# Kernel tuning notes

Hardware: AMD Instinct MI355X
Metric: run time of the kernel (lower is better)

Reference implementation:

```python
import jax, jax.numpy as jnp
import numpy as np

N = 4096
F_IN = 512
ALPHA = 0.2          # LeakyReLU negative slope
NEG_INF = -9e15      # mask fill used by pyGAT


def setup_inputs() -> dict:
    key = jax.random.key(0)
    ks = jax.random.split(key, 9)
    x = jax.random.normal(ks[0], (N, F_IN), dtype=jnp.float32)
    adj = (jax.random.uniform(ks[1], (N, N)) < 0.005).astype(jnp.float32)
    adj = jnp.maximum(adj, jnp.eye(N, dtype=jnp.float32))
    s = 0.05
    W1 = jax.random.normal(ks[2], (512, 8, 128), dtype=jnp.float32) * s
    a_src1 = jax.random.normal(ks[3], (8, 128), dtype=jnp.float32) * s
    a_dst1 = jax.random.normal(ks[4], (8, 128), dtype=jnp.float32) * s
    W2 = jax.random.normal(ks[5], (1024, 1, 16), dtype=jnp.float32) * s
    a_src2 = jax.random.normal(ks[6], (1, 16), dtype=jnp.float32) * s
    a_dst2 = jax.random.normal(ks[7], (1, 16), dtype=jnp.float32) * s
    return {"x": x, "adj": adj, "W1": W1, "a_src1": a_src1, "a_dst1": a_dst1,
            "W2": W2, "a_src2": a_src2, "a_dst2": a_dst2}


def gat_layer(x, mask, W, a_src, a_dst, concat, activation):
    # x: [N, Fin], W: [Fin, H, Fout]
    h = jnp.einsum('nf,fho->nho', x, W)                  # [N, H, Fout]
    f_src = jnp.einsum('nho,ho->hn', h, a_src)            # [H, N]
    f_dst = jnp.einsum('nho,ho->hn', h, a_dst)            # [H, N]
    e = f_src[:, :, None] + f_dst[:, None, :]             # [H, N, N]
    e = jax.nn.leaky_relu(e, ALPHA)
    e = jnp.where(mask[None, :, :], e, NEG_INF)
    attn = jax.nn.softmax(e, axis=-1)                     # masked softmax over neighbors j
    out = jnp.einsum('hij,jho->iho', attn, h)             # [N, H, Fout]
    if concat:
        out = out.reshape(out.shape[0], -1)               # [N, H*Fout]
    else:
        out = out.mean(axis=1)                            # [N, Fout]
    if activation:
        out = jax.nn.elu(out)
    return out


def reference(x, adj, W1, a_src1, a_dst1, W2, a_src2, a_dst2):
    mask = adj > 0
    h1 = gat_layer(x, mask, W1, a_src1, a_dst1, concat=True, activation=True)
    h2 = gat_layer(h1, mask, W2, a_src2, a_dst2, concat=False, activation=False)
    out = jax.nn.elu(h2)
    return jax.nn.log_softmax(out, axis=1)
```

## Files before the change

### kernel.cpp

```cpp
#include <hip/hip_runtime.h>
#include <hip/hip_bf16.h>
#include <hip/hip_fp16.h>

typedef __attribute__((ext_vector_type(8))) short short8;
typedef __attribute__((ext_vector_type(8))) _Float16 half8;
typedef __attribute__((ext_vector_type(2))) _Float16 h2v;
typedef __attribute__((ext_vector_type(4))) float f32x4;

#define MAXNBR 128
#define ALPHA 0.2f

static __device__ __forceinline__ unsigned short f2h(float f) {
    return __half_as_ushort(__float2half(f));
}
static __device__ __forceinline__ float h2f(unsigned short u) {
    return __half2float(__ushort_as_half(u));
}

__global__ __launch_bounds__(256) void cvt(const float* __restrict__ x,
                                           unsigned short* __restrict__ xh,
                                           const float* __restrict__ W1,
                                           unsigned short* __restrict__ W1t) {
    int b = blockIdx.x, t = threadIdx.x;
    if (b < 1024) {
        size_t base = (size_t)b * 2048 + t * 8;
        float4 v0 = *(const float4*)&x[base];
        float4 v1 = *(const float4*)&x[base + 4];
        short8 o;
        o[0] = f2h(v0.x); o[1] = f2h(v0.y); o[2] = f2h(v0.z); o[3] = f2h(v0.w);
        o[4] = f2h(v1.x); o[5] = f2h(v1.y); o[6] = f2h(v1.z); o[7] = f2h(v1.w);
        *(short8*)&xh[base] = o;
    } else {
        int idx = (b - 1024) * 256 + t;
        int c = idx >> 9, k = idx & 511;
        W1t[idx] = f2h(W1[(size_t)k * 1024 + c]);
    }
}

__global__ __launch_bounds__(256) void gemm_scan(const unsigned short* __restrict__ A,
                                                 const unsigned short* __restrict__ Bt,
                                                 unsigned short* __restrict__ C,
                                                 const float* __restrict__ adj,
                                                 int* __restrict__ nbr_idx,
                                                 int* __restrict__ nbr_cnt) {
    __shared__ unsigned short Asm[128 * 64];
    __shared__ unsigned short Bsm[64 * 64];
    int b = blockIdx.x;
    int tid = threadIdx.x;
    if (b < 512) {
        int lane = tid & 63;
        int w = tid >> 6;
        int wr = w >> 1, wc = w & 1;
        int rowBase = (b & 31) * 128, colBase = (b >> 5) * 64;
        int lr = lane >> 3;
        int lcs = ((lane & 7) ^ lr) * 8;
        f32x4 acc[4][2] = {};
        for (int k0 = 0; k0 < 512; k0 += 64) {
            #pragma unroll
            for (int i = 0; i < 4; ++i) {
                int rA = i * 32 + w * 8;
                __builtin_amdgcn_global_load_lds(
                    (const __attribute__((address_space(1))) void*)&A[(size_t)(rowBase + rA + lr) * 512 + k0 + lcs],
                    (__attribute__((address_space(3))) void*)&Asm[rA * 64],
                    16, 0, 0);
            }
            #pragma unroll
            for (int i = 0; i < 2; ++i) {
                int rB = i * 32 + w * 8;
                __builtin_amdgcn_global_load_lds(
                    (const __attribute__((address_space(1))) void*)&Bt[(size_t)(colBase + rB + lr) * 512 + k0 + lcs],
                    (__attribute__((address_space(3))) void*)&Bsm[rB * 64],
                    16, 0, 0);
            }
            __syncthreads();
            #pragma unroll
            for (int kk = 0; kk < 64; kk += 32) {
                half8 af[4], bfv[2];
                int kf = kk + (lane >> 4) * 8;
                #pragma unroll
                for (int m = 0; m < 4; ++m) {
                    int R = wr * 64 + m * 16 + (lane & 15);
                    af[m] = *(const half8*)&Asm[R * 64 + (kf ^ ((R & 7) << 3))];
                }
                #pragma unroll
                for (int n = 0; n < 2; ++n) {
                    int R = wc * 32 + n * 16 + (lane & 15);
                    bfv[n] = *(const half8*)&Bsm[R * 64 + (kf ^ ((R & 7) << 3))];
                }
                #pragma unroll
                for (int m = 0; m < 4; ++m)
                    #pragma unroll
                    for (int n = 0; n < 2; ++n)
                        acc[m][n] = __builtin_amdgcn_mfma_f32_16x16x32_f16(af[m], bfv[n], acc[m][n], 0, 0, 0);
            }
            __syncthreads();
        }
        int crow0 = rowBase + wr * 64, ccol0 = colBase + wc * 32;
        #pragma unroll
        for (int m = 0; m < 4; ++m)
            #pragma unroll
            for (int n = 0; n < 2; ++n) {
                int col = ccol0 + n * 16 + (lane & 15);
                int row0 = crow0 + m * 16 + (lane >> 4) * 4;
                #pragma unroll
                for (int r = 0; r < 4; ++r)
                    C[(size_t)(row0 + r) * 1024 + col] = f2h(acc[m][n][r]);
            }
    } else {
        int row = (b - 512) * 4 + (tid >> 6);
        int lane = tid & 63;
        const float* arow = adj + (size_t)row * 4096;
        int cnt = 0;
        for (int base = 0; base < 4096; base += 256) {
            float4 v = *(const float4*)&arow[base + lane * 4];
            #pragma unroll
            for (int s = 0; s < 4; ++s) {
                float xv = ((const float*)&v)[s];
                unsigned long long m = __ballot(xv > 0.f);
                if (xv > 0.f) {
                    int pos = cnt + (int)__popcll(m & ((1ull << lane) - 1ull));
                    if (pos < MAXNBR) nbr_idx[row * MAXNBR + pos] = base + lane * 4 + s;
                }
                cnt += (int)__popcll(m);
            }
        }
        if (lane == 0) nbr_cnt[row] = cnt < MAXNBR ? cnt : MAXNBR;
    }
}

__global__ __launch_bounds__(256) void attn_coef1(const unsigned short* __restrict__ h1h,
                                                  const float* __restrict__ a_src,
                                                  const float* __restrict__ a_dst,
                                                  float* __restrict__ fsp,
                                                  float* __restrict__ fdp) {
    int n = blockIdx.x, t = threadIdx.x;
    ushort4 v = *(const ushort4*)&h1h[(size_t)n * 1024 + t * 4];
    int head = t >> 5;
    int o0 = (t * 4) & 127;
    float hv0 = h2f(v.x), hv1 = h2f(v.y), hv2 = h2f(v.z), hv3 = h2f(v.w);
    float ps = hv0 * a_src[head * 128 + o0] + hv1 * a_src[head * 128 + o0 + 1]
             + hv2 * a_src[head * 128 + o0 + 2] + hv3 * a_src[head * 128 + o0 + 3];
    float pd = hv0 * a_dst[head * 128 + o0] + hv1 * a_dst[head * 128 + o0 + 1]
             + hv2 * a_dst[head * 128 + o0 + 2] + hv3 * a_dst[head * 128 + o0 + 3];
    #pragma unroll
    for (int off = 1; off < 32; off <<= 1) {
        ps += __shfl_xor(ps, off);
        pd += __shfl_xor(pd, off);
    }
    if ((t & 31) == 0) {
        fsp[n * 8 + head] = ps;
        fdp[n * 8 + head] = pd;
    }
}

__global__ __launch_bounds__(512) void aggregate6(const unsigned short* __restrict__ h1h,
                                                  const int* __restrict__ nbr_idx,
                                                  const int* __restrict__ nbr_cnt,
                                                  const float* __restrict__ fsp,
                                                  const float* __restrict__ fdp,
                                                  unsigned short* __restrict__ h1act) {
    __shared__ int nbr[MAXNBR];
    __shared__ float e_s[8][MAXNBR];
    __shared__ _Float16 attwS[8][MAXNBR];
    __shared__ half8 partS[3][128];
    int i = blockIdx.x;
    int t = threadIdx.x;
    int cnt = nbr_cnt[i];
    if (t < MAXNBR) nbr[t] = (t < cnt) ? nbr_idx[i * MAXNBR + t] : 0;
    __syncthreads();
    if (t < MAXNBR) {
        if (t < cnt) {
            int nb = nbr[t];
            float4 fs0 = *(const float4*)&fsp[i * 8];
            float4 fs1 = *(const float4*)&fsp[i * 8 + 4];
            float4 d0 = *(const float4*)&fdp[nb * 8];
            float4 d1 = *(const float4*)&fdp[nb * 8 + 4];
            float e0 = fs0.x + d0.x, e1 = fs0.y + d0.y, e2 = fs0.z + d0.z, e3 = fs0.w + d0.w;
            float e4 = fs1.x + d1.x, e5 = fs1.y + d1.y, e6 = fs1.z + d1.z, e7 = fs1.w + d1.w;
            e_s[0][t] = e0 > 0.f ? e0 : ALPHA * e0;
            e_s[1][t] = e1 > 0.f ? e1 : ALPHA * e1;
            e_s[2][t] = e2 > 0.f ? e2 : ALPHA * e2;
            e_s[3][t] = e3 > 0.f ? e3 : ALPHA * e3;
            e_s[4][t] = e4 > 0.f ? e4 : ALPHA * e4;
            e_s[5][t] = e5 > 0.f ? e5 : ALPHA * e5;
            e_s[6][t] = e6 > 0.f ? e6 : ALPHA * e6;
            e_s[7][t] = e7 > 0.f ? e7 : ALPHA * e7;
        } else {
            #pragma unroll
            for (int h = 0; h < 8; ++h) e_s[h][t] = -INFINITY;
        }
    }
    __syncthreads();
    if (t < 256) {
        int h = t >> 5, sl = t & 31;
        float e[4];
        #pragma unroll
        for (int p = 0; p < 4; ++p) e[p] = e_s[h][sl + p * 32];
        float m = fmaxf(fmaxf(e[0], e[1]), fmaxf(e[2], e[3]));
        #pragma unroll
        for (int off = 1; off < 32; off <<= 1) m = fmaxf(m, __shfl_xor(m, off));
        float wq[4], s = 0.f;
        #pragma unroll
        for (int p = 0; p < 4; ++p) {
            wq[p] = (e[p] == -INFINITY) ? 0.f : __expf(e[p] - m);
            s += wq[p];
        }
        #pragma unroll
        for (int off = 1; off < 32; off <<= 1) s += __shfl_xor(s, off);
        float inv = 1.f / s;
        #pragma unroll
        for (int p = 0; p < 4; ++p)
            attwS[h][sl + p * 32] = (_Float16)(wq[p] * inv);
    }
    __syncthreads();
    int tf = t & 127;
    int par = t >> 7;
    int head = tf >> 4;
    const unsigned short* src = h1h + tf * 8;
    h2v acc2[4] = {};
    int cntPad = (cnt + 3) & ~3;
    for (int j = par; j < cntPad; j += 4) {
        int nb = nbr[j];
        _Float16 wv = attwS[head][j];
        half8 v = *(const half8*)&src[(size_t)nb << 10];
        h2v wvv = (h2v){wv, wv};
        const h2v* pv = (const h2v*)&v;
        #pragma unroll
        for (int q = 0; q < 4; ++q)
            acc2[q] += wvv * pv[q];
    }
    if (par > 0) {
        half8 st;
        #pragma unroll
        for (int q = 0; q < 4; ++q) { st[q * 2] = acc2[q][0]; st[q * 2 + 1] = acc2[q][1]; }
        partS[par - 1][tf] = st;
    }
    __syncthreads();
    if (par == 0) {
        half8 p0 = partS[0][tf], p1 = partS[1][tf], p2 = partS[2][tf];
        short8 o;
        #pragma unroll
        for (int q = 0; q < 4; ++q) {
            float a0 = (float)acc2[q][0] + (float)p0[q * 2] + (float)p1[q * 2] + (float)p2[q * 2];
            float a1 = (float)acc2[q][1] + (float)p0[q * 2 + 1] + (float)p1[q * 2 + 1] + (float)p2[q * 2 + 1];
            a0 = a0 > 0.f ? a0 : (__expf(a0) - 1.f);
            a1 = a1 > 0.f ? a1 : (__expf(a1) - 1.f);
            o[q * 2] = f2h(a0);
            o[q * 2 + 1] = f2h(a1);
        }
        *(short8*)&h1act[(size_t)i * 1024 + tf * 8] = o;
    }
}

__global__ __launch_bounds__(256) void layer2_mfma(const unsigned short* __restrict__ h1act,
                                                   const float* __restrict__ W2,
                                                   const float* __restrict__ a_src2,
                                                   const float* __restrict__ a_dst2,
                                                   float* __restrict__ h2,
                                                   float2* __restrict__ fsd2) {
    __shared__ unsigned short W2t[16 * 1032];
    __shared__ float pred[4][256];
    int t = threadIdx.x, lane = t & 63, w = t >> 6;
    int rowBase = blockIdx.x * 16;
    for (int idx = t; idx < 16384; idx += 256) {
        int k = idx >> 4, o = idx & 15;
        W2t[o * 1032 + k] = f2h(W2[idx]);
    }
    __syncthreads();
    f32x4 acc = {};
    int r0 = lane & 15, kg = (lane >> 4) * 8;
    #pragma unroll
    for (int kk = 0; kk < 256; kk += 32) {
        int k0 = w * 256 + kk;
        half8 af = *(const half8*)&h1act[(size_t)(rowBase + r0) * 1024 + k0 + kg];
        half8 bf = *(const half8*)&W2t[r0 * 1032 + k0 + kg];
        acc = __builtin_amdgcn_mfma_f32_16x16x32_f16(af, bf, acc, 0, 0, 0);
    }
    #pragma unroll
    for (int r = 0; r < 4; ++r)
        pred[w][((lane >> 4) * 4 + r) * 16 + (lane & 15)] = acc[r];
    __syncthreads();
    if (t < 256) {
        int row = t >> 4, col = t & 15;
        float s = pred[0][t] + pred[1][t] + pred[2][t] + pred[3][t];
        h2[(rowBase + row) * 16 + col] = s;
        float ps = s * a_src2[col];
        float pd = s * a_dst2[col];
        #pragma unroll
        for (int off = 1; off < 16; off <<= 1) {
            ps += __shfl_xor(ps, off);
            pd += __shfl_xor(pd, off);
        }
        if (col == 0) fsd2[rowBase + row] = make_float2(ps, pd);
    }
}

__global__ __launch_bounds__(64) void final_layer(const float* __restrict__ h2,
                                                  const int* __restrict__ nbr_idx,
                                                  const int* __restrict__ nbr_cnt,
                                                  const float2* __restrict__ fsd2,
                                                  float* __restrict__ out) {
    __shared__ float attn[MAXNBR];
    __shared__ int nbr[MAXNBR];
    int i = blockIdx.x;
    int l = threadIdx.x;
    int cnt = nbr_cnt[i];
    float fsi = fsd2[i].x;
    for (int j = l; j < MAXNBR; j += 64) {
        float e = -INFINITY;
        if (j < cnt) {
            int jj = nbr_idx[i * MAXNBR + j];
            nbr[j] = jj;
            float xv = fsi + fsd2[jj].y;
            e = xv > 0.f ? xv : ALPHA * xv;
        }
        attn[j] = e;
    }
    __syncthreads();
    float m = fmaxf(attn[l], attn[l + 64]);
    #pragma unroll
    for (int off = 1; off < 64; off <<= 1) m = fmaxf(m, __shfl_xor(m, off));
    float s = 0.f;
    {
        float e0 = attn[l], e1 = attn[l + 64];
        if (e0 != -INFINITY) s += __expf(e0 - m);
        if (e1 != -INFINITY) s += __expf(e1 - m);
    }
    #pragma unroll
    for (int off = 1; off < 64; off <<= 1) s += __shfl_xor(s, off);
    for (int j = l; j < MAXNBR; j += 64) {
        float e = attn[j];
        attn[j] = (e == -INFINITY) ? 0.f : __expf(e - m) / s;
    }
    __syncthreads();
    if (l < 16) {
        float acc = 0.f;
        for (int j = 0; j < cnt; ++j)
            acc += attn[j] * h2[nbr[j] * 16 + l];
        float v = acc > 0.f ? acc : expm1f(acc);
        float mx = v;
        #pragma unroll
        for (int off = 1; off < 16; off <<= 1) mx = fmaxf(mx, __shfl_xor(mx, off));
        float se = __expf(v - mx);
        #pragma unroll
        for (int off = 1; off < 16; off <<= 1) se += __shfl_xor(se, off);
        out[i * 16 + l] = v - mx - logf(se);
    }
}

extern "C" void kernel_launch(void* const* d_in, const int* in_sizes, int n_in,
                              void* d_out, int out_size, void* d_ws, size_t ws_size,
                              hipStream_t stream) {
    const float* x      = (const float*)d_in[0];
    const float* adj    = (const float*)d_in[1];
    const float* W1     = (const float*)d_in[2];
    const float* a_src1 = (const float*)d_in[3];
    const float* a_dst1 = (const float*)d_in[4];
    const float* W2     = (const float*)d_in[5];
    const float* a_src2 = (const float*)d_in[6];
    const float* a_dst2 = (const float*)d_in[7];
    float* out = (float*)d_out;

    char* ws = (char*)d_ws;
    unsigned short* xh    = (unsigned short*)ws;
    unsigned short* w1t   = (unsigned short*)(ws + (4u << 20));
    unsigned short* h1h   = (unsigned short*)(ws + (6u << 20));
    float* fsp   = (float*)(ws + (14u << 20));
    float* fdp   = (float*)(ws + (14u << 20) + (128u << 10));
    float* h2    = (float*)(ws + (15u << 20));
    float2* fsd2 = (float2*)(ws + (15u << 20) + (256u << 10));
    int* nbr_idx = (int*)(ws + (16u << 20));
    int* nbr_cnt = (int*)(ws + (18u << 20));
    unsigned short* h1act = (unsigned short*)(ws + (26u << 20));

    cvt<<<3072, 256, 0, stream>>>(x, xh, W1, w1t);
    gemm_scan<<<1536, 256, 0, stream>>>(xh, w1t, h1h, adj, nbr_idx, nbr_cnt);
    attn_coef1<<<4096, 256, 0, stream>>>(h1h, a_src1, a_dst1, fsp, fdp);
    aggregate6<<<4096, 512, 0, stream>>>(h1h, nbr_idx, nbr_cnt, fsp, fdp, h1act);
    layer2_mfma<<<256, 256, 0, stream>>>(h1act, W2, a_src2, a_dst2, h2, fsd2);
    final_layer<<<4096, 64, 0, stream>>>(h2, nbr_idx, nbr_cnt, fsd2, out);
}
```

Baseline: 71.02 us.

## Tile W1 transpose through LDS and scan adjacency rows with block-wide prefix

The W1 transpose-and-convert now stages 64x64 tiles in padded shared memory, so both the global reads and the writes are coalesced instead of strided. This cuts the cvt grid from 3072 to 1152 blocks. The adjacency scan now gives each row a full 256-thread block: each thread loads 16 contiguous floats, builds a bitmask, and places neighbor indices using a wave shuffle prefix sum plus a cross-wave sum in shared memory. This replaces the serial 16-step ballot loop per wave but launches four times as many scan blocks, each with a barrier.

```diff
diff --git a/kernel.cpp b/kernel.cpp
--- a/kernel.cpp
+++ b/kernel.cpp
@@ -21,6 +21,7 @@
                                            unsigned short* __restrict__ xh,
                                            const float* __restrict__ W1,
                                            unsigned short* __restrict__ W1t) {
+    __shared__ float tile[64][65];
     int b = blockIdx.x, t = threadIdx.x;
     if (b < 1024) {
         size_t base = (size_t)b * 2048 + t * 8;
@@ -31,9 +32,16 @@
         o[4] = f2h(v1.x); o[5] = f2h(v1.y); o[6] = f2h(v1.z); o[7] = f2h(v1.w);
         *(short8*)&xh[base] = o;
     } else {
-        int idx = (b - 1024) * 256 + t;
-        int c = idx >> 9, k = idx & 511;
-        W1t[idx] = f2h(W1[(size_t)k * 1024 + c]);
+        int tb = b - 1024;
+        int tk = (tb >> 4) * 64, tc = (tb & 15) * 64;
+        int g = t >> 6, cx = t & 63;
+        #pragma unroll
+        for (int r = 0; r < 16; ++r)
+            tile[g * 16 + r][cx] = W1[(size_t)(tk + g * 16 + r) * 1024 + tc + cx];
+        __syncthreads();
+        #pragma unroll
+        for (int r = 0; r < 16; ++r)
+            W1t[(size_t)(tc + g * 16 + r) * 512 + tk + cx] = f2h(tile[cx][g * 16 + r]);
     }
 }
 
@@ -45,6 +53,7 @@
                                                  int* __restrict__ nbr_cnt) {
     __shared__ unsigned short Asm[128 * 64];
     __shared__ unsigned short Bsm[64 * 64];
+    __shared__ int wsum[4];
     int b = blockIdx.x;
     int tid = threadIdx.x;
     if (b < 512) {
@@ -107,24 +116,42 @@
                     C[(size_t)(row0 + r) * 1024 + col] = f2h(acc[m][n][r]);
             }
     } else {
-        int row = (b - 512) * 4 + (tid >> 6);
-        int lane = tid & 63;
+        int row = b - 512;
+        int t = tid;
         const float* arow = adj + (size_t)row * 4096;
-        int cnt = 0;
-        for (int base = 0; base < 4096; base += 256) {
-            float4 v = *(const float4*)&arow[base + lane * 4];
-            #pragma unroll
-            for (int s = 0; s < 4; ++s) {
-                float xv = ((const float*)&v)[s];
-                unsigned long long m = __ballot(xv > 0.f);
-                if (xv > 0.f) {
-                    int pos = cnt + (int)__popcll(m & ((1ull << lane) - 1ull));
-                    if (pos < MAXNBR) nbr_idx[row * MAXNBR + pos] = base + lane * 4 + s;
-                }
-                cnt += (int)__popcll(m);
+        const float4* ap = (const float4*)(arow + t * 16);
+        float4 v0 = ap[0], v1 = ap[1], v2 = ap[2], v3 = ap[3];
+        unsigned mask = 0;
+        #pragma unroll
+        for (int q = 0; q < 4; ++q) {
+            if (((const float*)&v0)[q] > 0.f) mask |= 1u << q;
+            if (((const float*)&v1)[q] > 0.f) mask |= 1u << (4 + q);
+            if (((const float*)&v2)[q] > 0.f) mask |= 1u << (8 + q);
+            if (((const float*)&v3)[q] > 0.f) mask |= 1u << (12 + q);
+        }
+        int mycnt = __popc(mask);
+        int lane = t & 63, w = t >> 6;
+        int incl = mycnt;
+        #pragma unroll
+        for (int d = 1; d < 64; d <<= 1) {
+            int nn = __shfl_up(incl, d);
+            if (lane >= d) incl += nn;
+        }
+        if (lane == 63) wsum[w] = incl;
+        __syncthreads();
+        int base = (w > 0 ? wsum[0] : 0) + (w > 1 ? wsum[1] : 0) + (w > 2 ? wsum[2] : 0);
+        int pos = base + incl - mycnt;
+        #pragma unroll
+        for (int q = 0; q < 16; ++q) {
+            if (mask & (1u << q)) {
+                if (pos < MAXNBR) nbr_idx[row * MAXNBR + pos] = t * 16 + q;
+                ++pos;
             }
         }
-        if (lane == 0) nbr_cnt[row] = cnt < MAXNBR ? cnt : MAXNBR;
+        if (t == 255) {
+            int tot = base + incl;
+            nbr_cnt[row] = tot < MAXNBR ? tot : MAXNBR;
+        }
     }
 }
 
@@ -373,8 +400,8 @@
     int* nbr_cnt = (int*)(ws + (18u << 20));
     unsigned short* h1act = (unsigned short*)(ws + (26u << 20));
 
-    cvt<<<3072, 256, 0, stream>>>(x, xh, W1, w1t);
-    gemm_scan<<<1536, 256, 0, stream>>>(xh, w1t, h1h, adj, nbr_idx, nbr_cnt);
+    cvt<<<1152, 256, 0, stream>>>(x, xh, W1, w1t);
+    gemm_scan<<<4608, 256, 0, stream>>>(xh, w1t, h1h, adj, nbr_idx, nbr_cnt);
     attn_coef1<<<4096, 256, 0, stream>>>(h1h, a_src1, a_dst1, fsp, fdp);
     aggregate6<<<4096, 512, 0, stream>>>(h1h, nbr_idx, nbr_cnt, fsp, fdp, h1act);
     layer2_mfma<<<256, 256, 0, stream>>>(h1act, W2, a_src2, a_dst2, h2, fsd2);
```

New measurement: 68.28 us. 1.04x faster.
